# Optimization experiments

Measured on AMD Instinct MI355X. Metric: run time of the kernel, lower is better.

## Reference

```python
import jax, jax.numpy as jnp
import numpy as np

NP, NA = 200000, 100000        # paper / author node counts
EW, EC = 300000, 300000        # writes / cites edge counts
HID, H, D = 128, 4, 32         # hidden, heads, head dim
FIN_P, FIN_A, OUT = 256, 128, 16
SCALE = float(1.0 / np.sqrt(D))


def _seg_softmax(alpha, idx, n):
    # softmax over edges grouped by destination node (PyG softmax)
    m = jax.ops.segment_max(alpha, idx, num_segments=n)
    e = jnp.exp(alpha - m[idx])
    s = jax.ops.segment_sum(e, idx, num_segments=n)
    return e / (s[idx] + 1e-16)


def _edge_type(k_src, v_src, q_dst, src, dst, a_rel, m_rel, p_rel, n_dst):
    # per-relation transform at node level, then gather-attend-scatter
    kr = jnp.einsum('nhd,hde->nhe', k_src, a_rel)
    vr = jnp.einsum('nhd,hde->nhe', v_src, m_rel)
    alpha = jnp.sum(q_dst[dst] * kr[src], axis=-1) * p_rel * SCALE  # [E,H]
    alpha = _seg_softmax(alpha, dst, n_dst)
    return jax.ops.segment_sum(vr[src] * alpha[..., None], dst, num_segments=n_dst)


def setup_inputs() -> dict:
    key = jax.random.key(0)
    ks = iter(jax.random.split(key, 48))

    def nrm(shape, s=0.05):
        return jax.random.normal(next(ks), shape, jnp.float32) * s

    inp = dict(
        x_paper=nrm((NP, FIN_P), 1.0),
        x_author=nrm((NA, FIN_A), 1.0),
        writes_src=jax.random.randint(next(ks), (EW,), 0, NA, dtype=jnp.int32),
        writes_dst=jax.random.randint(next(ks), (EW,), 0, NP, dtype=jnp.int32),
        cites_src=jax.random.randint(next(ks), (EC,), 0, NP, dtype=jnp.int32),
        cites_dst=jax.random.randint(next(ks), (EC,), 0, NP, dtype=jnp.int32),
        lin_paper_w=nrm((FIN_P, HID)), lin_paper_b=jnp.zeros((HID,), jnp.float32),
        lin_author_w=nrm((FIN_A, HID)), lin_author_b=jnp.zeros((HID,), jnp.float32),
        lin_out_w=nrm((HID, OUT)), lin_out_b=jnp.zeros((OUT,), jnp.float32),
    )
    for t in ('paper', 'author'):
        for nm in ('k', 'q', 'v', 'a'):
            inp[f'{nm}_w_{t}'] = nrm((HID, HID))
            inp[f'{nm}_b_{t}'] = jnp.zeros((HID,), jnp.float32)
        inp[f'skip_{t}'] = jnp.ones((), jnp.float32)
    for e in ('writes', 'cites'):
        inp[f'a_rel_{e}'] = nrm((H, D, D), 0.18)
        inp[f'm_rel_{e}'] = nrm((H, D, D), 0.18)
        inp[f'p_rel_{e}'] = jnp.ones((H,), jnp.float32)
    return inp


def reference(x_paper, x_author, writes_src, writes_dst, cites_src, cites_dst,
              lin_paper_w, lin_paper_b, lin_author_w, lin_author_b,
              lin_out_w, lin_out_b,
              k_w_paper, k_b_paper, q_w_paper, q_b_paper, v_w_paper, v_b_paper,
              a_w_paper, a_b_paper, skip_paper,
              k_w_author, k_b_author, q_w_author, q_b_author, v_w_author, v_b_author,
              a_w_author, a_b_author, skip_author,
              a_rel_writes, m_rel_writes, p_rel_writes,
              a_rel_cites, m_rel_cites, p_rel_cites):
    # per-node-type input projection + relu
    hp = jax.nn.relu(x_paper @ lin_paper_w + lin_paper_b)
    ha = jax.nn.relu(x_author @ lin_author_w + lin_author_b)
    # HGTConv: per-node-type k/q/v, [N,H,D]
    k_p = (hp @ k_w_paper + k_b_paper).reshape(NP, H, D)
    q_p = (hp @ q_w_paper + q_b_paper).reshape(NP, H, D)
    v_p = (hp @ v_w_paper + v_b_paper).reshape(NP, H, D)
    k_a = (ha @ k_w_author + k_b_author).reshape(NA, H, D)
    v_a = (ha @ v_w_author + v_b_author).reshape(NA, H, D)
    # heterogeneous multi-relation attention, group='sum' over edge types
    out_p = _edge_type(k_a, v_a, q_p, writes_src, writes_dst,
                       a_rel_writes, m_rel_writes, p_rel_writes, NP)
    out_p = out_p + _edge_type(k_p, v_p, q_p, cites_src, cites_dst,
                               a_rel_cites, m_rel_cites, p_rel_cites, NP)
    # output projection + gated skip (paper type; only 'paper' feeds the head)
    op = jax.nn.gelu(out_p.reshape(NP, HID), approximate=False) @ a_w_paper + a_b_paper
    beta = jax.nn.sigmoid(skip_paper)
    hp = beta * op + (1.0 - beta) * hp
    return hp @ lin_out_w + lin_out_b  # [NP, OUT]
```

## Files before the change

### kernel.cpp

```cpp
#include <hip/hip_runtime.h>
#include <cstdint>

#define NP 200000
#define NA 100000
#define EW 300000
#define EC 300000
#define HID 128
#define FIN_P 256
#define FIN_A 128
#define NOUT 16
#define ATT_SCALE 0.17677669529663687f

#define NBP 1563
#define NBA 782

#define SCAN_N (2 * NP)
#define SCAN_BS 256
#define SCAN_ITEMS 4
#define SCAN_TILE 1024
#define SCAN_NB ((SCAN_N + SCAN_TILE - 1) / SCAN_TILE)

typedef short s8v __attribute__((ext_vector_type(8)));
typedef float f32x4 __attribute__((ext_vector_type(4)));
typedef unsigned short ushort_t;

__device__ __forceinline__ float gelu_f(float x) {
  return 0.5f * x * (1.0f + erff(x * 0.70710678118654752f));
}
__device__ __forceinline__ ushort_t f2bf(float f) {
  unsigned u = __float_as_uint(f);
  return (ushort_t)((u + 0x7FFFu + ((u >> 16) & 1u)) >> 16);
}
__device__ __forceinline__ unsigned pack2bf(float a, float b) {
  return (unsigned)f2bf(a) | ((unsigned)f2bf(b) << 16);
}
__device__ __forceinline__ float bflo(unsigned u) { return __uint_as_float(u << 16); }
__device__ __forceinline__ float bfhi(unsigned u) { return __uint_as_float(u & 0xFFFF0000u); }

__device__ __forceinline__ void gl16(const void* g, void* l) {
  __builtin_amdgcn_global_load_lds(
      (const __attribute__((address_space(1))) void*)g,
      (__attribute__((address_space(3))) void*)l, 16, 0, 0);
}

__global__ void prep_all(
    const float* __restrict__ qw,  const float* __restrict__ qb,
    const float* __restrict__ kwp, const float* __restrict__ kbp, const float* __restrict__ arc,
    const float* __restrict__ vwp, const float* __restrict__ vbp, const float* __restrict__ mrc,
    const float* __restrict__ kwa, const float* __restrict__ kba, const float* __restrict__ arw,
    const float* __restrict__ vwa, const float* __restrict__ vba, const float* __restrict__ mrw,
    const float* __restrict__ lpw, const float* __restrict__ law,
    const float* __restrict__ aw, const float* __restrict__ ab,
    const float* __restrict__ skip, const float* __restrict__ W2, const float* __restrict__ b2,
    ushort_t* __restrict__ Wall, float* __restrict__ Ball,
    float* __restrict__ Wg, float* __restrict__ Wh, float* __restrict__ bo,
    int* __restrict__ cnt)
{
  const int b = blockIdx.x, tid = threadIdx.x;
  if (b == 0) {
    for (int idx = tid; idx < 16384; idx += 256) {
      int c = idx >> 7, r = idx & 127;
      Wall[idx] = f2bf(qw[r * 128 + c]);
    }
    for (int c = tid; c < 128; c += 256) Ball[c] = qb[c];
  } else if (b <= 4) {
    const float *W, *bias, *rel;
    switch (b) {
      case 1:  W = kwp; bias = kbp; rel = arc; break;
      case 2:  W = vwp; bias = vbp; rel = mrc; break;
      case 3:  W = kwa; bias = kba; rel = arw; break;
      default: W = vwa; bias = vba; rel = mrw; break;
    }
    for (int idx = tid; idx < 16384; idx += 256) {
      int c = idx >> 7, r = idx & 127, h = c >> 5, e = c & 31;
      float s = 0.f;
      #pragma unroll
      for (int d = 0; d < 32; ++d) s += W[r * 128 + h * 32 + d] * rel[h * 1024 + d * 32 + e];
      Wall[b * 16384 + idx] = f2bf(s);
    }
    for (int c = tid; c < 128; c += 256) {
      int h = c >> 5, e = c & 31;
      float s = 0.f;
      #pragma unroll
      for (int d = 0; d < 32; ++d) s += bias[h * 32 + d] * rel[h * 1024 + d * 32 + e];
      Ball[b * 128 + c] = s;
    }
  } else if (b == 5) {
    for (int idx = tid; idx < 16384; idx += 256) {
      int c = idx >> 7, r = idx & 127;
      Wall[5 * 16384 + idx] = f2bf(law[r * 128 + c]);
    }
  } else if (b == 6) {
    for (int idx = tid; idx < 32768; idx += 256) {
      int c = idx >> 8, r = idx & 255;
      Wall[6 * 16384 + idx] = f2bf(lpw[r * 128 + c]);
    }
  } else if (b == 7) {
    float beta = 1.0f / (1.0f + expf(-skip[0]));
    for (int idx = tid; idx < 128 * 16; idx += 256) {
      int r = idx >> 4, c = idx & 15;
      float s = 0.f;
      for (int k = 0; k < 128; ++k) s += aw[r * 128 + k] * W2[k * 16 + c];
      Wg[idx] = beta * s;
      Wh[idx] = (1.0f - beta) * W2[idx];
    }
    if (tid < 16) {
      float s = 0.f;
      for (int k = 0; k < 128; ++k) s += ab[k] * W2[k * 16 + tid];
      bo[tid] = beta * s + b2[tid];
    }
  } else {
    int chunk = SCAN_N / 8;
    int base = (b - 8) * chunk;
    for (int i = tid; i < chunk; i += 256) cnt[base + i] = 0;
  }
}

__global__ __launch_bounds__(256) void gemm_proj(
    const float* __restrict__ xp, const float* __restrict__ xa,
    const ushort_t* __restrict__ Wall,
    const float* __restrict__ bp, const float* __restrict__ ba,
    ushort_t* __restrict__ hpo, ushort_t* __restrict__ hao)
{
  __shared__ ushort_t As[4][128][8];
  __shared__ ushort_t Bs[4][128][8];
  const bool isP = blockIdx.x < NBP;
  const int bid = isP ? blockIdx.x : blockIdx.x - NBP;
  const float* A = isP ? xp : xa;
  const ushort_t* W = Wall + (isP ? 6 * 16384 : 5 * 16384);
  const float* bias = isP ? bp : ba;
  ushort_t* C = isP ? hpo : hao;
  const int M = isP ? NP : NA;
  const int KT = isP ? 256 : 128;

  const int tid  = threadIdx.x;
  const int lane = tid & 63;
  const int wv   = tid >> 6;
  const int wr   = wv >> 1, wc = wv & 1;
  const int l15  = lane & 15, kgl = lane >> 4;
  const int row0 = bid * 128;

  f32x4 acc[4][4];
  #pragma unroll
  for (int i = 0; i < 4; ++i)
    #pragma unroll
    for (int j = 0; j < 4; ++j) acc[i][j] = (f32x4){0.f, 0.f, 0.f, 0.f};

  for (int kt = 0; kt < KT; kt += 32) {
    #pragma unroll
    for (int half = 0; half < 2; ++half) {
      int slot = half * 256 + tid;
      int kg = slot >> 7, r = slot & 127;
      int grow = row0 + r; if (grow > M - 1) grow = M - 1;
      const float* ga = A + (size_t)grow * KT + kt + kg * 8;
      float4 a0 = *(const float4*)ga;
      float4 a1 = *(const float4*)(ga + 4);
      uint4 v;
      v.x = pack2bf(a0.x, a0.y); v.y = pack2bf(a0.z, a0.w);
      v.z = pack2bf(a1.x, a1.y); v.w = pack2bf(a1.z, a1.w);
      *(uint4*)&As[kg][r][0] = v;
    }
    #pragma unroll
    for (int half = 0; half < 2; ++half) {
      int slot = half * 256 + tid;
      int kg = slot >> 7, c = slot & 127;
      gl16(W + (size_t)c * KT + kt + kg * 8, &Bs[kg][c][0]);
    }
    __syncthreads();

    const s8v* As8 = (const s8v*)&As[0][0][0];
    const s8v* Bs8 = (const s8v*)&Bs[0][0][0];
    s8v af[4], bfv[4];
    #pragma unroll
    for (int i = 0; i < 4; ++i) af[i]  = As8[kgl * 128 + wr * 64 + i * 16 + l15];
    #pragma unroll
    for (int j = 0; j < 4; ++j) bfv[j] = Bs8[kgl * 128 + wc * 64 + j * 16 + l15];
    #pragma unroll
    for (int i = 0; i < 4; ++i)
      #pragma unroll
      for (int j = 0; j < 4; ++j)
        acc[i][j] = __builtin_amdgcn_mfma_f32_16x16x32_bf16(af[i], bfv[j], acc[i][j], 0, 0, 0);
    __syncthreads();
  }

  float bv[4];
  #pragma unroll
  for (int j = 0; j < 4; ++j) bv[j] = bias[wc * 64 + j * 16 + l15];
  #pragma unroll
  for (int i = 0; i < 4; ++i) {
    #pragma unroll
    for (int r = 0; r < 4; ++r) {
      int row = row0 + wr * 64 + i * 16 + kgl * 4 + r;
      if (row < M) {
        #pragma unroll
        for (int j = 0; j < 4; ++j) {
          float v = acc[i][j][r] + bv[j];
          v = fmaxf(v, 0.f);
          C[(size_t)row * 128 + wc * 64 + j * 16 + l15] = f2bf(v);
        }
      }
    }
  }
}

__global__ __launch_bounds__(256) void gemm_kv(
    const ushort_t* __restrict__ hpA, const ushort_t* __restrict__ haA,
    const ushort_t* __restrict__ Wall, const float* __restrict__ Ball,
    ushort_t* __restrict__ qkv, ushort_t* __restrict__ kvw)
{
  __shared__ ushort_t As[4][128][8];
  __shared__ ushort_t Bs[4][128][8];
  int b = blockIdx.x;
  int set, bid, M;
  const ushort_t* A;
  ushort_t* C;
  if (b < 3 * NBP) {
    set = b / NBP; bid = b - set * NBP;
    A = hpA; M = NP;
    C = qkv + (size_t)set * NP * HID;
  } else {
    int t = b - 3 * NBP;
    int s2 = t / NBA; bid = t - s2 * NBA;
    set = 3 + s2;
    A = haA; M = NA;
    C = kvw + (size_t)s2 * NA * HID;
  }
  const ushort_t* W = Wall + set * 16384;
  const float* bias = Ball + set * 128;

  const int tid  = threadIdx.x;
  const int lane = tid & 63;
  const int wv   = tid >> 6;
  const int wr   = wv >> 1, wc = wv & 1;
  const int l15  = lane & 15, kgl = lane >> 4;
  const int row0 = bid * 128;

  f32x4 acc[4][4];
  #pragma unroll
  for (int i = 0; i < 4; ++i)
    #pragma unroll
    for (int j = 0; j < 4; ++j) acc[i][j] = (f32x4){0.f, 0.f, 0.f, 0.f};

  #pragma unroll
  for (int kt = 0; kt < 128; kt += 32) {
    #pragma unroll
    for (int half = 0; half < 2; ++half) {
      int slot = half * 256 + tid;
      int kg = slot >> 7, r = slot & 127;
      int grow = row0 + r; if (grow > M - 1) grow = M - 1;
      gl16(A + (size_t)grow * 128 + kt + kg * 8, &As[kg][r][0]);
    }
    #pragma unroll
    for (int half = 0; half < 2; ++half) {
      int slot = half * 256 + tid;
      int kg = slot >> 7, c = slot & 127;
      gl16(W + (size_t)c * 128 + kt + kg * 8, &Bs[kg][c][0]);
    }
    __syncthreads();

    const s8v* As8 = (const s8v*)&As[0][0][0];
    const s8v* Bs8 = (const s8v*)&Bs[0][0][0];
    s8v af[4], bfv[4];
    #pragma unroll
    for (int i = 0; i < 4; ++i) af[i]  = As8[kgl * 128 + wr * 64 + i * 16 + l15];
    #pragma unroll
    for (int j = 0; j < 4; ++j) bfv[j] = Bs8[kgl * 128 + wc * 64 + j * 16 + l15];
    #pragma unroll
    for (int i = 0; i < 4; ++i)
      #pragma unroll
      for (int j = 0; j < 4; ++j)
        acc[i][j] = __builtin_amdgcn_mfma_f32_16x16x32_bf16(af[i], bfv[j], acc[i][j], 0, 0, 0);
    __syncthreads();
  }

  float bv[4];
  #pragma unroll
  for (int j = 0; j < 4; ++j) bv[j] = bias[wc * 64 + j * 16 + l15];
  #pragma unroll
  for (int i = 0; i < 4; ++i) {
    #pragma unroll
    for (int r = 0; r < 4; ++r) {
      int row = row0 + wr * 64 + i * 16 + kgl * 4 + r;
      if (row < M) {
        #pragma unroll
        for (int j = 0; j < 4; ++j) {
          C[(size_t)row * 128 + wc * 64 + j * 16 + l15] = f2bf(acc[i][j][r] + bv[j]);
        }
      }
    }
  }
}

__global__ void hist_k(const int* __restrict__ wdst, const int* __restrict__ cdst,
                       int* __restrict__ cnt)
{
  int t = blockIdx.x * blockDim.x + threadIdx.x;
  if (t < EW) atomicAdd(&cnt[wdst[t]], 1);
  if (t < EC) atomicAdd(&cnt[NP + cdst[t]], 1);
}

__global__ __launch_bounds__(SCAN_BS) void scan1(const int* __restrict__ cnt,
                                                 int* __restrict__ off,
                                                 int* __restrict__ bsum)
{
  __shared__ int sh[2][SCAN_BS];
  int tid = threadIdx.x;
  int base = blockIdx.x * SCAN_TILE + tid * SCAN_ITEMS;
  int v[SCAN_ITEMS]; int tsum = 0;
  #pragma unroll
  for (int i = 0; i < SCAN_ITEMS; ++i) {
    int idx = base + i;
    v[i] = (idx < SCAN_N) ? cnt[idx] : 0;
    tsum += v[i];
  }
  int p = 0;
  sh[0][tid] = tsum; __syncthreads();
  #pragma unroll
  for (int d = 1; d < SCAN_BS; d <<= 1) {
    int x = sh[p][tid] + ((tid >= d) ? sh[p][tid - d] : 0);
    sh[p ^ 1][tid] = x; __syncthreads(); p ^= 1;
  }
  int run = sh[p][tid] - tsum;
  #pragma unroll
  for (int i = 0; i < SCAN_ITEMS; ++i) {
    int idx = base + i;
    if (idx < SCAN_N) off[idx] = run;
    run += v[i];
  }
  if (tid == SCAN_BS - 1) bsum[blockIdx.x] = sh[p][tid];
}

__global__ __launch_bounds__(512) void scan2(int* __restrict__ bsum)
{
  __shared__ int sh[2][512];
  int tid = threadIdx.x;
  int v = (tid < SCAN_NB) ? bsum[tid] : 0;
  int p = 0;
  sh[0][tid] = v; __syncthreads();
  for (int d = 1; d < 512; d <<= 1) {
    int x = sh[p][tid] + ((tid >= d) ? sh[p][tid - d] : 0);
    sh[p ^ 1][tid] = x; __syncthreads(); p ^= 1;
  }
  if (tid < SCAN_NB) bsum[tid] = sh[p][tid] - v;
}

__global__ __launch_bounds__(SCAN_BS) void scan3(int* __restrict__ off, int* __restrict__ cur,
                                                 const int* __restrict__ bsum)
{
  int add = bsum[blockIdx.x];
  int base = blockIdx.x * SCAN_TILE + threadIdx.x;
  #pragma unroll
  for (int i = 0; i < SCAN_ITEMS; ++i) {
    int idx = base + i * SCAN_BS;
    if (idx < SCAN_N) { int t = off[idx] + add; off[idx] = t; cur[idx] = t; }
  }
  if (blockIdx.x == 0 && threadIdx.x == 0) off[SCAN_N] = EW + EC;
}

__global__ void fill_k(const int* __restrict__ wsrc, const int* __restrict__ wdst,
                       const int* __restrict__ csrc, const int* __restrict__ cdst,
                       int* __restrict__ cur, int* __restrict__ esrc)
{
  int t = blockIdx.x * blockDim.x + threadIdx.x;
  if (t < EW) { int p = atomicAdd(&cur[wdst[t]], 1); esrc[p] = wsrc[t] << 8; }
  if (t < EC) { int p = atomicAdd(&cur[NP + cdst[t]], 1); esrc[p] = csrc[t] << 8; }
}

__global__ __launch_bounds__(256) void node_attn(
    const int* __restrict__ off, const int* __restrict__ esrc,
    const ushort_t* __restrict__ q,
    const ushort_t* __restrict__ kr_w, const ushort_t* __restrict__ vr_w,
    const ushort_t* __restrict__ kr_c, const ushort_t* __restrict__ vr_c,
    const float* __restrict__ p_rel_w, const float* __restrict__ p_rel_c,
    ushort_t* __restrict__ out_p)
{
  int gid = blockIdx.x * blockDim.x + threadIdx.x;
  int node = gid >> 4;
  int l16 = gid & 15;
  int h = l16 >> 2;

  uint4 qv = *(const uint4*)(q + (size_t)node * HID + l16 * 8);
  float qf[8];
  {
    const unsigned* pq = (const unsigned*)&qv;
    #pragma unroll
    for (int w = 0; w < 4; ++w) { qf[2 * w] = bflo(pq[w]); qf[2 * w + 1] = bfhi(pq[w]); }
  }
  float prw = p_rel_w[h] * ATT_SCALE;
  float prc = p_rel_c[h] * ATT_SCALE;
  unsigned loff = (unsigned)(l16 * 16);

  float t[8];
  #pragma unroll
  for (int i = 0; i < 8; ++i) t[i] = 0.f;

  #pragma unroll
  for (int r = 0; r < 2; ++r) {
    const char* krb = (const char*)((r == 0) ? kr_w : kr_c);
    const char* vrb = (const char*)((r == 0) ? vr_w : vr_c);
    float prr = (r == 0) ? prw : prc;
    int eb = off[(r == 0 ? 0 : NP) + node];
    int ee = off[(r == 0 ? 0 : NP) + node + 1];

    float s = 0.f;
    float A[8];
    #pragma unroll
    for (int i = 0; i < 8; ++i) A[i] = 0.f;

    for (int e = eb; e < ee; ++e) {
      unsigned kb = (unsigned)esrc[e] + loff;
      uint4 kv = *(const uint4*)(krb + kb);
      uint4 vv = *(const uint4*)(vrb + kb);
      const unsigned* pk = (const unsigned*)&kv;
      float d = 0.f;
      #pragma unroll
      for (int w = 0; w < 4; ++w) {
        d = fmaf(qf[2 * w], bflo(pk[w]), d);
        d = fmaf(qf[2 * w + 1], bfhi(pk[w]), d);
      }
      d += __shfl_xor(d, 1);
      d += __shfl_xor(d, 2);
      float p = __expf(d * prr);
      s += p;
      const unsigned* pv = (const unsigned*)&vv;
      #pragma unroll
      for (int w = 0; w < 4; ++w) {
        A[2 * w]     = fmaf(p, bflo(pv[w]), A[2 * w]);
        A[2 * w + 1] = fmaf(p, bfhi(pv[w]), A[2 * w + 1]);
      }
    }
    float inv = 1.0f / (s + 1e-16f);
    #pragma unroll
    for (int i = 0; i < 8; ++i) t[i] = fmaf(A[i], inv, t[i]);
  }

  uint4 o;
  unsigned* po = (unsigned*)&o;
  #pragma unroll
  for (int w = 0; w < 4; ++w) po[w] = pack2bf(t[2 * w], t[2 * w + 1]);
  *(uint4*)(out_p + (size_t)node * HID + l16 * 8) = o;
}

__global__ __launch_bounds__(256) void epilogue_k(
    const ushort_t* __restrict__ out_p, const ushort_t* __restrict__ hp,
    const float* __restrict__ Wg, const float* __restrict__ Wh,
    const float* __restrict__ bo, float* __restrict__ out)
{
  __shared__ float Ts[64][129];
  __shared__ float Wgs[128][16];
  __shared__ float Whs[128][16];
  __shared__ float bs[16];
  int tid = threadIdx.x;
  int row0 = blockIdx.x * 64;

  #pragma unroll
  for (int i = 0; i < 2; ++i) {
    int idx = tid + i * 256;
    *(float4*)&Wgs[idx >> 2][(idx & 3) << 2] = *(const float4*)(Wg + (size_t)idx * 4);
    *(float4*)&Whs[idx >> 2][(idx & 3) << 2] = *(const float4*)(Wh + (size_t)idx * 4);
  }
  if (tid < 16) bs[tid] = bo[tid];

  #pragma unroll
  for (int i = 0; i < 4; ++i) {
    int idx = tid + i * 256;
    int r = idx >> 4, c8 = (idx & 15) << 3;
    uint4 g = *(const uint4*)(out_p + (size_t)(row0 + r) * HID + c8);
    const unsigned* pw = (const unsigned*)&g;
    #pragma unroll
    for (int w = 0; w < 4; ++w) {
      Ts[r][c8 + 2 * w]     = gelu_f(bflo(pw[w]));
      Ts[r][c8 + 2 * w + 1] = gelu_f(bfhi(pw[w]));
    }
  }
  __syncthreads();

  int row = tid & 63, cg = tid >> 6;
  float acc[4];
  #pragma unroll
  for (int j = 0; j < 4; ++j) acc[j] = bs[cg * 4 + j];
  for (int k = 0; k < 128; ++k) {
    float g = Ts[row][k];
    float4 w = *(const float4*)&Wgs[k][cg << 2];
    acc[0] = fmaf(g, w.x, acc[0]); acc[1] = fmaf(g, w.y, acc[1]);
    acc[2] = fmaf(g, w.z, acc[2]); acc[3] = fmaf(g, w.w, acc[3]);
  }
  __syncthreads();

  #pragma unroll
  for (int i = 0; i < 4; ++i) {
    int idx = tid + i * 256;
    int r = idx >> 4, c8 = (idx & 15) << 3;
    uint4 hh = *(const uint4*)(hp + (size_t)(row0 + r) * HID + c8);
    const unsigned* pw = (const unsigned*)&hh;
    #pragma unroll
    for (int w = 0; w < 4; ++w) {
      Ts[r][c8 + 2 * w]     = bflo(pw[w]);
      Ts[r][c8 + 2 * w + 1] = bfhi(pw[w]);
    }
  }
  __syncthreads();
  for (int k = 0; k < 128; ++k) {
    float hv = Ts[row][k];
    float4 w = *(const float4*)&Whs[k][cg << 2];
    acc[0] = fmaf(hv, w.x, acc[0]); acc[1] = fmaf(hv, w.y, acc[1]);
    acc[2] = fmaf(hv, w.z, acc[2]); acc[3] = fmaf(hv, w.w, acc[3]);
  }
  *(float4*)(out + (size_t)(row0 + row) * NOUT + (cg << 2)) =
      make_float4(acc[0], acc[1], acc[2], acc[3]);
}

extern "C" void kernel_launch(void* const* d_in, const int* in_sizes, int n_in,
                              void* d_out, int out_size, void* d_ws, size_t ws_size,
                              hipStream_t stream)
{
  (void)in_sizes; (void)n_in; (void)out_size; (void)ws_size;
  const float* x_paper      = (const float*)d_in[0];
  const float* x_author     = (const float*)d_in[1];
  const int*   writes_src   = (const int*)d_in[2];
  const int*   writes_dst   = (const int*)d_in[3];
  const int*   cites_src    = (const int*)d_in[4];
  const int*   cites_dst    = (const int*)d_in[5];
  const float* lin_paper_w  = (const float*)d_in[6];
  const float* lin_paper_b  = (const float*)d_in[7];
  const float* lin_author_w = (const float*)d_in[8];
  const float* lin_author_b = (const float*)d_in[9];
  const float* lin_out_w    = (const float*)d_in[10];
  const float* lin_out_b    = (const float*)d_in[11];
  const float* k_w_paper    = (const float*)d_in[12];
  const float* k_b_paper    = (const float*)d_in[13];
  const float* q_w_paper    = (const float*)d_in[14];
  const float* q_b_paper    = (const float*)d_in[15];
  const float* v_w_paper    = (const float*)d_in[16];
  const float* v_b_paper    = (const float*)d_in[17];
  const float* a_w_paper    = (const float*)d_in[18];
  const float* a_b_paper    = (const float*)d_in[19];
  const float* skip_paper   = (const float*)d_in[20];
  const float* k_w_author   = (const float*)d_in[21];
  const float* k_b_author   = (const float*)d_in[22];
  const float* v_w_author   = (const float*)d_in[25];
  const float* v_b_author   = (const float*)d_in[26];
  const float* a_rel_writes = (const float*)d_in[30];
  const float* m_rel_writes = (const float*)d_in[31];
  const float* p_rel_writes = (const float*)d_in[32];
  const float* a_rel_cites  = (const float*)d_in[33];
  const float* m_rel_cites  = (const float*)d_in[34];
  const float* p_rel_cites  = (const float*)d_in[35];

  float* ws = (float*)d_ws;
  size_t off_f = 0;
  auto nxt = [&](size_t nfloats) { float* p = ws + off_f; off_f += nfloats; return p; };
  ushort_t* hp    = (ushort_t*)nxt((size_t)NP * 64);
  ushort_t* ha    = (ushort_t*)nxt((size_t)NA * 64);
  ushort_t* qkv   = (ushort_t*)nxt((size_t)3 * NP * 64);
  ushort_t* kvw   = (ushort_t*)nxt((size_t)2 * NA * 64);
  ushort_t* outp  = (ushort_t*)nxt((size_t)NP * 64);
  int*      cnt   = (int*)nxt(SCAN_N);
  int*      offs  = (int*)nxt(SCAN_N + 2);
  int*      cur   = (int*)nxt(SCAN_N);
  int*      esrc  = (int*)nxt(EW + EC);
  int*      bsum  = (int*)nxt(512);
  ushort_t* Wall  = (ushort_t*)nxt(65536);
  float*    Ball  = nxt(5 * 128);
  float*    Wg    = nxt(2048);
  float*    Wh    = nxt(2048);
  float*    bo    = nxt(16);

  ushort_t* q_p  = qkv;
  ushort_t* kr_c = qkv + (size_t)NP * HID;
  ushort_t* vr_c = qkv + (size_t)2 * NP * HID;
  ushort_t* kr_w = kvw;
  ushort_t* vr_w = kvw + (size_t)NA * HID;

  prep_all<<<16, 256, 0, stream>>>(q_w_paper, q_b_paper,
                                   k_w_paper, k_b_paper, a_rel_cites,
                                   v_w_paper, v_b_paper, m_rel_cites,
                                   k_w_author, k_b_author, a_rel_writes,
                                   v_w_author, v_b_author, m_rel_writes,
                                   lin_paper_w, lin_author_w,
                                   a_w_paper, a_b_paper, skip_paper, lin_out_w, lin_out_b,
                                   Wall, Ball, Wg, Wh, bo, cnt);

  hist_k<<<(300000 + 255) / 256, 256, 0, stream>>>(writes_dst, cites_dst, cnt);
  scan1<<<SCAN_NB, SCAN_BS, 0, stream>>>(cnt, offs, bsum);
  scan2<<<1, 512, 0, stream>>>(bsum);
  scan3<<<SCAN_NB, SCAN_BS, 0, stream>>>(offs, cur, bsum);
  fill_k<<<(300000 + 255) / 256, 256, 0, stream>>>(writes_src, writes_dst,
                                                   cites_src, cites_dst, cur, esrc);

  gemm_proj<<<NBP + NBA, 256, 0, stream>>>(x_paper, x_author, Wall,
                                           lin_paper_b, lin_author_b, hp, ha);
  gemm_kv<<<3 * NBP + 2 * NBA, 256, 0, stream>>>(hp, ha, Wall, Ball, qkv, kvw);

  node_attn<<<(NP * 16) / 256, 256, 0, stream>>>(
      offs, esrc, q_p, kr_w, vr_w, kr_c, vr_c, p_rel_writes, p_rel_cites, outp);

  epilogue_k<<<(NP + 63) / 64, 256, 0, stream>>>(outp, hp, Wg, Wh, bo, (float*)d_out);
}
```

Measured before the change: 462.4 us.

## Double-buffer LDS tiles in projection GEMMs with register prefetch

Both projection GEMM kernels now keep two LDS buffers. The next K-slice is loaded into registers before the current MFMA block runs, then written to the other buffer, so each iteration needs one barrier instead of two and global latency overlaps compute. The direct global-to-LDS loads are replaced by register-staged loads with coalesced row/k-group mapping, and fp32-to-bf16 packing uses the hardware packed convert instruction instead of manual rounding. This doubles LDS use per block and adds register pressure, which may lower occupancy.

```diff
diff --git a/kernel.cpp b/kernel.cpp
--- a/kernel.cpp
+++ b/kernel.cpp
@@ -34,14 +34,13 @@
 __device__ __forceinline__ unsigned pack2bf(float a, float b) {
   return (unsigned)f2bf(a) | ((unsigned)f2bf(b) << 16);
 }
+__device__ __forceinline__ unsigned cvtpk(float a, float b) {
+  unsigned r;
+  asm("v_cvt_pk_bf16_f32 %0, %1, %2" : "=v"(r) : "v"(a), "v"(b));
+  return r;
+}
 __device__ __forceinline__ float bflo(unsigned u) { return __uint_as_float(u << 16); }
 __device__ __forceinline__ float bfhi(unsigned u) { return __uint_as_float(u & 0xFFFF0000u); }
-
-__device__ __forceinline__ void gl16(const void* g, void* l) {
-  __builtin_amdgcn_global_load_lds(
-      (const __attribute__((address_space(1))) void*)g,
-      (__attribute__((address_space(3))) void*)l, 16, 0, 0);
-}
 
 __global__ void prep_all(
     const float* __restrict__ qw,  const float* __restrict__ qb,
@@ -122,8 +121,8 @@
     const float* __restrict__ bp, const float* __restrict__ ba,
     ushort_t* __restrict__ hpo, ushort_t* __restrict__ hao)
 {
-  __shared__ ushort_t As[4][128][8];
-  __shared__ ushort_t Bs[4][128][8];
+  __shared__ ushort_t As[2][4][128][8];
+  __shared__ ushort_t Bs[2][4][128][8];
   const bool isP = blockIdx.x < NBP;
   const int bid = isP ? blockIdx.x : blockIdx.x - NBP;
   const float* A = isP ? xp : xa;
@@ -132,6 +131,7 @@
   ushort_t* C = isP ? hpo : hao;
   const int M = isP ? NP : NA;
   const int KT = isP ? 256 : 128;
+  const int nt = KT >> 5;
 
   const int tid  = threadIdx.x;
   const int lane = tid & 63;
@@ -140,36 +140,50 @@
   const int l15  = lane & 15, kgl = lane >> 4;
   const int row0 = bid * 128;
 
+  const int r0 = tid >> 2, kg0 = tid & 3;
+  int g0 = row0 + r0;       if (g0 > M - 1) g0 = M - 1;
+  int g1 = row0 + r0 + 64;  if (g1 > M - 1) g1 = M - 1;
+  const float* a0p = A + (size_t)g0 * KT + kg0 * 8;
+  const float* a1p = A + (size_t)g1 * KT + kg0 * 8;
+  const ushort_t* b0p = W + (size_t)r0 * KT + kg0 * 8;
+  const ushort_t* b1p = W + (size_t)(r0 + 64) * KT + kg0 * 8;
+
+  float4 fa[4];
+  uint4 rb[2];
+  auto stage = [&](int kt) {
+    fa[0] = *(const float4*)(a0p + kt); fa[1] = *(const float4*)(a0p + kt + 4);
+    fa[2] = *(const float4*)(a1p + kt); fa[3] = *(const float4*)(a1p + kt + 4);
+    rb[0] = *(const uint4*)(b0p + kt);  rb[1] = *(const uint4*)(b1p + kt);
+  };
+  auto commit = [&](int buf) {
+    uint4 v0, v1;
+    v0.x = cvtpk(fa[0].x, fa[0].y); v0.y = cvtpk(fa[0].z, fa[0].w);
+    v0.z = cvtpk(fa[1].x, fa[1].y); v0.w = cvtpk(fa[1].z, fa[1].w);
+    v1.x = cvtpk(fa[2].x, fa[2].y); v1.y = cvtpk(fa[2].z, fa[2].w);
+    v1.z = cvtpk(fa[3].x, fa[3].y); v1.w = cvtpk(fa[3].z, fa[3].w);
+    *(uint4*)&As[buf][kg0][r0][0]      = v0;
+    *(uint4*)&As[buf][kg0][r0 + 64][0] = v1;
+    *(uint4*)&Bs[buf][kg0][r0][0]      = rb[0];
+    *(uint4*)&Bs[buf][kg0][r0 + 64][0] = rb[1];
+  };
+
   f32x4 acc[4][4];
   #pragma unroll
   for (int i = 0; i < 4; ++i)
     #pragma unroll
     for (int j = 0; j < 4; ++j) acc[i][j] = (f32x4){0.f, 0.f, 0.f, 0.f};
 
-  for (int kt = 0; kt < KT; kt += 32) {
-    #pragma unroll
-    for (int half = 0; half < 2; ++half) {
-      int slot = half * 256 + tid;
-      int kg = slot >> 7, r = slot & 127;
-      int grow = row0 + r; if (grow > M - 1) grow = M - 1;
-      const float* ga = A + (size_t)grow * KT + kt + kg * 8;
-      float4 a0 = *(const float4*)ga;
-      float4 a1 = *(const float4*)(ga + 4);
-      uint4 v;
-      v.x = pack2bf(a0.x, a0.y); v.y = pack2bf(a0.z, a0.w);
-      v.z = pack2bf(a1.x, a1.y); v.w = pack2bf(a1.z, a1.w);
-      *(uint4*)&As[kg][r][0] = v;
-    }
-    #pragma unroll
-    for (int half = 0; half < 2; ++half) {
-      int slot = half * 256 + tid;
-      int kg = slot >> 7, c = slot & 127;
-      gl16(W + (size_t)c * KT + kt + kg * 8, &Bs[kg][c][0]);
-    }
-    __syncthreads();
-
-    const s8v* As8 = (const s8v*)&As[0][0][0];
-    const s8v* Bs8 = (const s8v*)&Bs[0][0][0];
+  stage(0);
+  commit(0);
+  __syncthreads();
+  int cur = 0;
+
+  for (int t = 0; t < nt; ++t) {
+    bool more = (t + 1) < nt;
+    if (more) stage((t + 1) * 32);
+
+    const s8v* As8 = (const s8v*)&As[cur][0][0][0];
+    const s8v* Bs8 = (const s8v*)&Bs[cur][0][0][0];
     s8v af[4], bfv[4];
     #pragma unroll
     for (int i = 0; i < 4; ++i) af[i]  = As8[kgl * 128 + wr * 64 + i * 16 + l15];
@@ -180,7 +194,12 @@
       #pragma unroll
       for (int j = 0; j < 4; ++j)
         acc[i][j] = __builtin_amdgcn_mfma_f32_16x16x32_bf16(af[i], bfv[j], acc[i][j], 0, 0, 0);
-    __syncthreads();
+
+    if (more) {
+      commit(cur ^ 1);
+      __syncthreads();
+      cur ^= 1;
+    }
   }
 
   float bv[4];
@@ -208,8 +227,8 @@
     const ushort_t* __restrict__ Wall, const float* __restrict__ Ball,
     ushort_t* __restrict__ qkv, ushort_t* __restrict__ kvw)
 {
-  __shared__ ushort_t As[4][128][8];
-  __shared__ ushort_t Bs[4][128][8];
+  __shared__ ushort_t As[2][4][128][8];
+  __shared__ ushort_t Bs[2][4][128][8];
   int b = blockIdx.x;
   int set, bid, M;
   const ushort_t* A;
@@ -235,31 +254,44 @@
   const int l15  = lane & 15, kgl = lane >> 4;
   const int row0 = bid * 128;
 
+  const int r0 = tid >> 2, kg0 = tid & 3;
+  int g0 = row0 + r0;       if (g0 > M - 1) g0 = M - 1;
+  int g1 = row0 + r0 + 64;  if (g1 > M - 1) g1 = M - 1;
+  const ushort_t* a0p = A + (size_t)g0 * 128 + kg0 * 8;
+  const ushort_t* a1p = A + (size_t)g1 * 128 + kg0 * 8;
+  const ushort_t* b0p = W + (size_t)r0 * 128 + kg0 * 8;
+  const ushort_t* b1p = W + (size_t)(r0 + 64) * 128 + kg0 * 8;
+
+  uint4 ra[2], rb[2];
+  auto stage = [&](int kt) {
+    ra[0] = *(const uint4*)(a0p + kt); ra[1] = *(const uint4*)(a1p + kt);
+    rb[0] = *(const uint4*)(b0p + kt); rb[1] = *(const uint4*)(b1p + kt);
+  };
+  auto commit = [&](int buf) {
+    *(uint4*)&As[buf][kg0][r0][0]      = ra[0];
+    *(uint4*)&As[buf][kg0][r0 + 64][0] = ra[1];
+    *(uint4*)&Bs[buf][kg0][r0][0]      = rb[0];
+    *(uint4*)&Bs[buf][kg0][r0 + 64][0] = rb[1];
+  };
+
   f32x4 acc[4][4];
   #pragma unroll
   for (int i = 0; i < 4; ++i)
     #pragma unroll
     for (int j = 0; j < 4; ++j) acc[i][j] = (f32x4){0.f, 0.f, 0.f, 0.f};
 
-  #pragma unroll
-  for (int kt = 0; kt < 128; kt += 32) {
-    #pragma unroll
-    for (int half = 0; half < 2; ++half) {
-      int slot = half * 256 + tid;
-      int kg = slot >> 7, r = slot & 127;
-      int grow = row0 + r; if (grow > M - 1) grow = M - 1;
-      gl16(A + (size_t)grow * 128 + kt + kg * 8, &As[kg][r][0]);
-    }
-    #pragma unroll
-    for (int half = 0; half < 2; ++half) {
-      int slot = half * 256 + tid;
-      int kg = slot >> 7, c = slot & 127;
-      gl16(W + (size_t)c * 128 + kt + kg * 8, &Bs[kg][c][0]);
-    }
-    __syncthreads();
-
-    const s8v* As8 = (const s8v*)&As[0][0][0];
-    const s8v* Bs8 = (const s8v*)&Bs[0][0][0];
+  stage(0);
+  commit(0);
+  __syncthreads();
+  int cur = 0;
+
+  #pragma unroll
+  for (int t = 0; t < 4; ++t) {
+    bool more = (t + 1) < 4;
+    if (more) stage((t + 1) * 32);
+
+    const s8v* As8 = (const s8v*)&As[cur][0][0][0];
+    const s8v* Bs8 = (const s8v*)&Bs[cur][0][0][0];
     s8v af[4], bfv[4];
     #pragma unroll
     for (int i = 0; i < 4; ++i) af[i]  = As8[kgl * 128 + wr * 64 + i * 16 + l15];
@@ -270,7 +302,12 @@
       #pragma unroll
       for (int j = 0; j < 4; ++j)
         acc[i][j] = __builtin_amdgcn_mfma_f32_16x16x32_bf16(af[i], bfv[j], acc[i][j], 0, 0, 0);
-    __syncthreads();
+
+    if (more) {
+      commit(cur ^ 1);
+      __syncthreads();
+      cur ^= 1;
+    }
   }
 
   float bv[4];
```

Result: slower. 507.2 us (+9.7%).
